# Kernel tuning notes

Measured on AMD Instinct MI355X. Metric: run time of the kernel, lower is better.

The kernel has to match this reference:

```python
import jax, jax.numpy as jnp
import numpy as np

N_NODES = 100000
N_EDGES = 1000000
EMB = 64
HID = 64
N_CLASSES = 1
LEAKY_SLOPE = 0.01  # flax.linen.leaky_relu default


def setup_inputs() -> dict:
    key = jax.random.key(0)
    k1, k2, k3, k4, k5 = jax.random.split(key, 5)
    node_ids = jnp.arange(N_NODES, dtype=jnp.int32)
    senders = jax.random.randint(k1, (N_EDGES,), 0, N_NODES, dtype=jnp.int32)
    receivers = jax.random.randint(k2, (N_EDGES,), 0, N_NODES, dtype=jnp.int32)
    embed_table = jax.random.normal(k3, (N_NODES, EMB), dtype=jnp.float32) * 0.05
    W1 = jax.random.normal(k4, (EMB, HID), dtype=jnp.float32) * (1.0 / np.sqrt(EMB))
    W2 = jax.random.normal(k5, (HID, N_CLASSES), dtype=jnp.float32) * (1.0 / np.sqrt(HID))
    b2 = jnp.zeros((N_CLASSES,), dtype=jnp.float32)
    return {"node_ids": node_ids, "senders": senders, "receivers": receivers,
            "embed_table": embed_table, "W1": W1, "W2": W2, "b2": b2}


def gcn_aggregate(x, senders, receivers, n_nodes, symmetric):
    # Faithful to jraph.GraphConvolution: update_node_fn is applied BEFORE this.
    if symmetric:
        ones = jnp.ones_like(senders, dtype=x.dtype)
        send_deg = jax.ops.segment_sum(ones, senders, num_segments=n_nodes)
        recv_deg = jax.ops.segment_sum(ones, receivers, num_segments=n_nodes)
        x = x * jax.lax.rsqrt(jnp.maximum(send_deg, 1.0))[:, None]
        x = jax.ops.segment_sum(x[senders], receivers, num_segments=n_nodes)  # [N, d]
        x = x * jax.lax.rsqrt(jnp.maximum(recv_deg, 1.0))[:, None]
    else:
        x = jax.ops.segment_sum(x[senders], receivers, num_segments=n_nodes)
    return x


def reference(node_ids, senders, receivers, embed_table, W1, W2, b2):
    n = node_ids.shape[0]
    # GraphMapFeatures(embed_node_fn=nn.Embed(...))
    x = embed_table[node_ids]                      # [N, EMB]
    # GraphConvolution(Dense(hidden, use_bias=False), symmetric_normalization=True)
    x = x @ W1                                     # [N, HID]
    x = gcn_aggregate(x, senders, receivers, n, symmetric=True)
    x = jax.nn.leaky_relu(x, negative_slope=LEAKY_SLOPE)
    # GraphConvolution(Dense(classes), symmetric_normalization=False)
    x = x @ W2 + b2                                # [N, C]
    x = gcn_aggregate(x, senders, receivers, n, symmetric=False)
    return jax.nn.sigmoid(x)
```

## Files before the change

kernel.cpp:

```cpp
#include <hip/hip_runtime.h>
#include <hip/hip_bf16.h>

#define N_NODES 100000
#define N_EDGES 1000000
#define SCAN_B 256
#define N_BLOCKS_RS ((N_NODES + 255) / 256)
#define N_BLOCKS_A  ((N_NODES + 63) / 64)

#define CHUNKS 40
#define CHUNK_E 25000
#define HWORDS 25000
#define HIST_BLOCKS (2 * CHUNKS)
#define MLP_BLOCKS 176
#define MLP_WAVES (MLP_BLOCKS * 16)


__device__ __forceinline__ unsigned f32_to_bf16(float v) {
    unsigned u = __float_as_uint(v);
    return (u + 0x7fffu + ((u >> 16) & 1u)) >> 16;
}

__global__ void k_hist8_mlp(const int4* __restrict__ s4,
                            const int4* __restrict__ r4,
                            unsigned* __restrict__ ghist_s8,
                            unsigned* __restrict__ ghist_r8,
                            unsigned char* __restrict__ rank8,
                            const float* __restrict__ emb,
                            const float* __restrict__ W1,
                            unsigned short* __restrict__ h16) {
    __shared__ unsigned lds[HWORDS];
    int b = blockIdx.x;
    int t = threadIdx.x;

    if (b >= HIST_BLOCKS) {
        int lane = t & 63;
        int gw   = (b - HIST_BLOCKS) * 16 + (t >> 6);
        float w1c[64];
#pragma unroll
        for (int k = 0; k < 64; ++k) w1c[k] = W1[k * 64 + lane];

        for (int n = gw; n < N_NODES; n += MLP_WAVES) {
            float e = emb[(size_t)n * 64 + lane];
            float a0 = 0.f, a1 = 0.f, a2 = 0.f, a3 = 0.f;
            int ei = __float_as_int(e);
#pragma unroll
            for (int k = 0; k < 16; ++k) {
                a0 += __int_as_float(__builtin_amdgcn_readlane(ei, 4 * k + 0)) * w1c[4 * k + 0];
                a1 += __int_as_float(__builtin_amdgcn_readlane(ei, 4 * k + 1)) * w1c[4 * k + 1];
                a2 += __int_as_float(__builtin_amdgcn_readlane(ei, 4 * k + 2)) * w1c[4 * k + 2];
                a3 += __int_as_float(__builtin_amdgcn_readlane(ei, 4 * k + 3)) * w1c[4 * k + 3];
            }
            float a = (a0 + a1) + (a2 + a3);
            h16[(size_t)n * 64 + lane] = (unsigned short)f32_to_bf16(a);
        }
        return;
    }

    int isR = (b < CHUNKS);
    int c   = isR ? b : b - CHUNKS;

    for (int w = t; w < HWORDS; w += 1024) lds[w] = 0u;
    __syncthreads();

    int beg = c * (CHUNK_E / 4);
    int end = beg + CHUNK_E / 4;
    if (isR) {
        for (int q = beg + t; q < end; q += 1024) {
            int4 v = r4[q];
            int sh0 = (v.x & 3) * 8, sh1 = (v.y & 3) * 8;
            int sh2 = (v.z & 3) * 8, sh3 = (v.w & 3) * 8;
            unsigned o0 = atomicAdd(&lds[v.x >> 2], 1u << sh0);
            unsigned o1 = atomicAdd(&lds[v.y >> 2], 1u << sh1);
            unsigned o2 = atomicAdd(&lds[v.z >> 2], 1u << sh2);
            unsigned o3 = atomicAdd(&lds[v.w >> 2], 1u << sh3);
            uchar4 rk;
            rk.x = (unsigned char)((o0 >> sh0) & 0xffu);
            rk.y = (unsigned char)((o1 >> sh1) & 0xffu);
            rk.z = (unsigned char)((o2 >> sh2) & 0xffu);
            rk.w = (unsigned char)((o3 >> sh3) & 0xffu);
            *(uchar4*)(rank8 + 4 * (size_t)q) = rk;
        }
    } else {
        for (int q = beg + t; q < end; q += 1024) {
            int4 v = s4[q];
            atomicAdd(&lds[v.x >> 2], 1u << ((v.x & 3) * 8));
            atomicAdd(&lds[v.y >> 2], 1u << ((v.y & 3) * 8));
            atomicAdd(&lds[v.z >> 2], 1u << ((v.z & 3) * 8));
            atomicAdd(&lds[v.w >> 2], 1u << ((v.w & 3) * 8));
        }
    }
    __syncthreads();

    uint4* __restrict__ dst =
        (uint4*)((isR ? ghist_r8 : ghist_s8) + (size_t)c * HWORDS);
    const uint4* lsrc = (const uint4*)lds;
    for (int w = t; w < HWORDS / 4; w += 1024) dst[w] = lsrc[w];
}

__global__ void k_scanA(const unsigned char* __restrict__ gs8,
                        const unsigned char* __restrict__ gr8,
                        unsigned char* __restrict__ base8,
                        int* __restrict__ part,
                        float* __restrict__ rs,
                        int* __restrict__ blockSums) {
    __shared__ int s[64];
    int t = threadIdx.x;
    int g = t >> 2, sl = t & 3;
    int node = blockIdx.x * 64 + g;
    int total = 0;
    if (node < N_NODES) {
        unsigned ss = 0;
#pragma unroll
        for (int k = 0; k < 10; ++k)
            ss += gs8[(size_t)(sl * 10 + k) * N_NODES + node];
        ss += __shfl_xor(ss, 1, 64);
        ss += __shfl_xor(ss, 2, 64);
        if (sl == 0) rs[node] = rsqrtf(fmaxf((float)ss, 1.0f));

        unsigned rv[10];
        unsigned rsum = 0;
#pragma unroll
        for (int k = 0; k < 10; ++k) {
            rv[k] = gr8[(size_t)(sl * 10 + k) * N_NODES + node];
            rsum += rv[k];
        }
        unsigned x = rsum;
        unsigned u1 = __shfl_up(x, 1, 4); if (sl >= 1) x += u1;
        unsigned u2 = __shfl_up(x, 2, 4); if (sl >= 2) x += u2;
        unsigned run = x - rsum;
        total = (int)__shfl(x, 3, 4);
#pragma unroll
        for (int k = 0; k < 10; ++k) {
            base8[(size_t)(sl * 10 + k) * N_NODES + node] = (unsigned char)run;
            run += rv[k];
        }
    }
    if (sl == 0) s[g] = total;
    __syncthreads();
    if (t < 64) {
        int v = s[t];
        int acc = v;
#pragma unroll
        for (int off = 1; off < 64; off <<= 1) {
            int y = __shfl_up(acc, off, 64);
            if (t >= off) acc += y;
        }
        s[t] = acc - v;
        if (t == 63) blockSums[blockIdx.x] = acc;
    }
    __syncthreads();
    if (sl == 0 && node < N_NODES) part[node] = s[g];
}

__global__ void k_rows(const int* __restrict__ part,
                       const int* __restrict__ blockSums,
                       int* __restrict__ row_start) {
    __shared__ int s[SCAN_B];
    __shared__ int gsum[4];
    int t = threadIdx.x;
    int b = blockIdx.x;

    int acc = 0;
    for (int j = t; j < 4 * b; j += SCAN_B) acc += blockSums[j];
    s[t] = acc;
    __syncthreads();
    for (int off = SCAN_B / 2; off > 0; off >>= 1) {
        if (t < off) s[t] += s[t + off];
        __syncthreads();
    }
    int blockOff = s[0];
    if (t < 4)
        gsum[t] = (4 * b + t < N_BLOCKS_A) ? blockSums[4 * b + t] : 0;
    __syncthreads();

    int gi = t >> 6;
    int goff = blockOff;
    if (gi > 0) goff += gsum[0];
    if (gi > 1) goff += gsum[1];
    if (gi > 2) goff += gsum[2];
    int n = b * SCAN_B + t;
    if (n < N_NODES) row_start[n] = goff + part[n];
    if (b == 0 && t == 0) row_start[N_NODES] = N_EDGES;
}

__global__ void k_fill(const int4* __restrict__ s4,
                       const int4* __restrict__ r4,
                       const uchar4* __restrict__ rk4,
                       const unsigned char* __restrict__ base8,
                       const int* __restrict__ row_start,
                       int* __restrict__ col) {
    int i = blockIdx.x * blockDim.x + threadIdx.x;
    if (i >= N_EDGES / 4) return;
    int c = (4 * i) / CHUNK_E;
    const unsigned char* __restrict__ bs = base8 + (size_t)c * N_NODES;
    int4 s = s4[i];
    int4 r = r4[i];
    uchar4 rk = rk4[i];
    col[row_start[r.x] + bs[r.x] + rk.x] = s.x;
    col[row_start[r.y] + bs[r.y] + rk.y] = s.y;
    col[row_start[r.z] + bs[r.z] + rk.z] = s.z;
    col[row_start[r.w] + bs[r.w] + rk.w] = s.w;
}

__global__ void k_agg_post(const int* __restrict__ row_start,
                           const int* __restrict__ col,
                           const uint4* __restrict__ h128,
                           const float* __restrict__ rs,
                           const float* __restrict__ W2,
                           const float* __restrict__ b2,
                           float* __restrict__ z) {
    int wid  = (blockIdx.x * blockDim.x + threadIdx.x) >> 6;
    int lane = threadIdx.x & 63;
    if (wid >= N_NODES) return;
    int eslot = lane >> 3;
    int fq    = lane & 7;

    int start = row_start[wid];
    int end   = row_start[wid + 1];
    float a0 = 0.f, a1 = 0.f, a2 = 0.f, a3 = 0.f;
    float a4 = 0.f, a5 = 0.f, a6 = 0.f, a7 = 0.f;
    for (int i = start + eslot; i < end; i += 8) {
        int sx = col[i];
        float rss = rs[sx];
        uint4 u = h128[(size_t)sx * 8 + fq];
        a0 += rss * __uint_as_float(u.x << 16);
        a1 += rss * __uint_as_float(u.x & 0xffff0000u);
        a2 += rss * __uint_as_float(u.y << 16);
        a3 += rss * __uint_as_float(u.y & 0xffff0000u);
        a4 += rss * __uint_as_float(u.z << 16);
        a5 += rss * __uint_as_float(u.z & 0xffff0000u);
        a6 += rss * __uint_as_float(u.w << 16);
        a7 += rss * __uint_as_float(u.w & 0xffff0000u);
    }
#pragma unroll
    for (int off = 8; off < 64; off <<= 1) {
        a0 += __shfl_xor(a0, off, 64);
        a1 += __shfl_xor(a1, off, 64);
        a2 += __shfl_xor(a2, off, 64);
        a3 += __shfl_xor(a3, off, 64);
        a4 += __shfl_xor(a4, off, 64);
        a5 += __shfl_xor(a5, off, 64);
        a6 += __shfl_xor(a6, off, 64);
        a7 += __shfl_xor(a7, off, 64);
    }
    float rsq = rsqrtf(fmaxf((float)(end - start), 1.0f));
    float4 wA = ((const float4*)W2)[fq * 2];
    float4 wB = ((const float4*)W2)[fq * 2 + 1];
    float p = 0.f, x;
    x = a0 * rsq; x = (x > 0.f) ? x : 0.01f * x; p += x * wA.x;
    x = a1 * rsq; x = (x > 0.f) ? x : 0.01f * x; p += x * wA.y;
    x = a2 * rsq; x = (x > 0.f) ? x : 0.01f * x; p += x * wA.z;
    x = a3 * rsq; x = (x > 0.f) ? x : 0.01f * x; p += x * wA.w;
    x = a4 * rsq; x = (x > 0.f) ? x : 0.01f * x; p += x * wB.x;
    x = a5 * rsq; x = (x > 0.f) ? x : 0.01f * x; p += x * wB.y;
    x = a6 * rsq; x = (x > 0.f) ? x : 0.01f * x; p += x * wB.z;
    x = a7 * rsq; x = (x > 0.f) ? x : 0.01f * x; p += x * wB.w;
    p += __shfl_xor(p, 1, 64);
    p += __shfl_xor(p, 2, 64);
    p += __shfl_xor(p, 4, 64);
    if (lane == 0) z[wid] = p + b2[0];
}

__global__ void k_agg2_sigmoid(const int* __restrict__ row_start,
                               const int* __restrict__ col,
                               const float* __restrict__ z,
                               float* __restrict__ out) {
    int gtid = blockIdx.x * blockDim.x + threadIdx.x;
    int n  = gtid >> 2;
    int sl = gtid & 3;
    if (n >= N_NODES) return;
    int start = row_start[n];
    int end   = row_start[n + 1];
    float acc = 0.f;
    for (int i = start + sl; i < end; i += 4) acc += z[col[i]];
    acc += __shfl_xor(acc, 1, 64);
    acc += __shfl_xor(acc, 2, 64);
    if (sl == 0) out[n] = 1.0f / (1.0f + expf(-acc));
}

extern "C" void kernel_launch(void* const* d_in, const int* in_sizes, int n_in,
                              void* d_out, int out_size, void* d_ws, size_t ws_size,
                              hipStream_t stream) {
    const int* senders    = (const int*)d_in[1];
    const int* receivers  = (const int*)d_in[2];
    const float* emb      = (const float*)d_in[3];
    const float* W1       = (const float*)d_in[4];
    const float* W2       = (const float*)d_in[5];
    const float* b2       = (const float*)d_in[6];
    float* out            = (float*)d_out;

    char* ws = (char*)d_ws;
    unsigned char*  ghist_s8  = (unsigned char*)(ws);
    unsigned char*  ghist_r8  = (unsigned char*)(ws + 4000000);
    unsigned char*  base8     = (unsigned char*)(ws + 8000000);
    unsigned char*  rank8     = (unsigned char*)(ws + 12000000);
    int*            part      = (int*)(ws + 13000000);
    int*            row_start = (int*)(ws + 13400000);
    int*            blockSums = (int*)(ws + 13800016);
    float*          rs        = (float*)(ws + 13807600);
    int*            col       = (int*)(ws + 14207600);
    unsigned short* h16       = (unsigned short*)(ws + 18207616);
    float*          z         = (float*)(ws + 31007616);

    const int B = 256;
    const int QBLK = (N_EDGES / 4 + B - 1) / B;

    k_hist8_mlp<<<HIST_BLOCKS + MLP_BLOCKS, 1024, 0, stream>>>(
        (const int4*)senders, (const int4*)receivers,
        (unsigned*)ghist_s8, (unsigned*)ghist_r8, rank8, emb, W1, h16);
    k_scanA<<<N_BLOCKS_A, B, 0, stream>>>(
        ghist_s8, ghist_r8, base8, part, rs, blockSums);
    k_rows<<<N_BLOCKS_RS, SCAN_B, 0, stream>>>(part, blockSums, row_start);
    k_fill<<<QBLK, B, 0, stream>>>(
        (const int4*)senders, (const int4*)receivers,
        (const uchar4*)rank8, base8, row_start, col);
    k_agg_post<<<(N_NODES * 64) / B, B, 0, stream>>>(
        row_start, col, (const uint4*)h16, rs, W2, b2, z);
    k_agg2_sigmoid<<<(N_NODES * 4 + B - 1) / B, B, 0, stream>>>(
        row_start, col, z, out);
}
```

Before: 190.1 us.

## Fuse CSR build stages into one cooperative kernel with grid syncs

Merges the histogram/MLP, scan, row-offset and fill kernels into a single cooperative kernel of 256 blocks that uses grid.sync between phases, removing three kernel launches and their inter-kernel gaps. The scan is restructured so each lane handles a whole node across all 40 chunks, followed by a single-block scan of group sums. The fill phase computes offsets from groupOff+part directly instead of reading row_start. The risks are grid-sync overhead, the fixed 256-block grid limiting parallelism for the fill, and the requirement that all blocks be co-resident.

Result: slower. 299.3 us (+57.5%).

```diff
diff --git a/kernel.cpp b/kernel.cpp
--- a/kernel.cpp
+++ b/kernel.cpp
@@ -1,11 +1,11 @@
 #include <hip/hip_runtime.h>
+#include <hip/hip_cooperative_groups.h>
 #include <hip/hip_bf16.h>
+
+namespace cg = cooperative_groups;
 
 #define N_NODES 100000
 #define N_EDGES 1000000
-#define SCAN_B 256
-#define N_BLOCKS_RS ((N_NODES + 255) / 256)
-#define N_BLOCKS_A  ((N_NODES + 63) / 64)
 
 #define CHUNKS 40
 #define CHUNK_E 25000
@@ -13,6 +13,8 @@
 #define HIST_BLOCKS (2 * CHUNKS)
 #define MLP_BLOCKS 176
 #define MLP_WAVES (MLP_BLOCKS * 16)
+#define NG 1563
+#define GRID_THREADS (256 * 1024)
 
 
 __device__ __forceinline__ unsigned f32_to_bf16(float v) {
@@ -20,25 +22,65 @@
     return (u + 0x7fffu + ((u >> 16) & 1u)) >> 16;
 }
 
-__global__ void k_hist8_mlp(const int4* __restrict__ s4,
-                            const int4* __restrict__ r4,
-                            unsigned* __restrict__ ghist_s8,
-                            unsigned* __restrict__ ghist_r8,
-                            unsigned char* __restrict__ rank8,
-                            const float* __restrict__ emb,
-                            const float* __restrict__ W1,
-                            unsigned short* __restrict__ h16) {
-    __shared__ unsigned lds[HWORDS];
+__global__ void __launch_bounds__(1024, 1)
+k_build(const int4* __restrict__ s4, const int4* __restrict__ r4,
+        unsigned char* __restrict__ ghist_s8,
+        unsigned char* __restrict__ ghist_r8,
+        unsigned char* __restrict__ rank8,
+        const float* __restrict__ emb, const float* __restrict__ W1,
+        unsigned short* __restrict__ h16,
+        unsigned char* __restrict__ base8,
+        int* __restrict__ part, float* __restrict__ rs,
+        int* __restrict__ blockSums, int* __restrict__ groupOff,
+        int* __restrict__ row_start, int* __restrict__ col) {
+    __shared__ unsigned lds[HWORDS + 600];
+    cg::grid_group grid = cg::this_grid();
     int b = blockIdx.x;
     int t = threadIdx.x;
 
-    if (b >= HIST_BLOCKS) {
+    if (b < HIST_BLOCKS) {
+        int isR = (b < CHUNKS);
+        int c   = isR ? b : b - CHUNKS;
+        for (int w = t; w < HWORDS; w += 1024) lds[w] = 0u;
+        __syncthreads();
+        int beg = c * (CHUNK_E / 4);
+        int end = beg + CHUNK_E / 4;
+        if (isR) {
+            for (int q = beg + t; q < end; q += 1024) {
+                int4 v = r4[q];
+                int sh0 = (v.x & 3) * 8, sh1 = (v.y & 3) * 8;
+                int sh2 = (v.z & 3) * 8, sh3 = (v.w & 3) * 8;
+                unsigned o0 = atomicAdd(&lds[v.x >> 2], 1u << sh0);
+                unsigned o1 = atomicAdd(&lds[v.y >> 2], 1u << sh1);
+                unsigned o2 = atomicAdd(&lds[v.z >> 2], 1u << sh2);
+                unsigned o3 = atomicAdd(&lds[v.w >> 2], 1u << sh3);
+                uchar4 rk;
+                rk.x = (unsigned char)((o0 >> sh0) & 0xffu);
+                rk.y = (unsigned char)((o1 >> sh1) & 0xffu);
+                rk.z = (unsigned char)((o2 >> sh2) & 0xffu);
+                rk.w = (unsigned char)((o3 >> sh3) & 0xffu);
+                *(uchar4*)(rank8 + 4 * (size_t)q) = rk;
+            }
+        } else {
+            for (int q = beg + t; q < end; q += 1024) {
+                int4 v = s4[q];
+                atomicAdd(&lds[v.x >> 2], 1u << ((v.x & 3) * 8));
+                atomicAdd(&lds[v.y >> 2], 1u << ((v.y & 3) * 8));
+                atomicAdd(&lds[v.z >> 2], 1u << ((v.z & 3) * 8));
+                atomicAdd(&lds[v.w >> 2], 1u << ((v.w & 3) * 8));
+            }
+        }
+        __syncthreads();
+        uint4* __restrict__ dst =
+            (uint4*)((isR ? ghist_r8 : ghist_s8) + (size_t)c * HWORDS * 4);
+        const uint4* lsrc = (const uint4*)lds;
+        for (int w = t; w < HWORDS / 4; w += 1024) dst[w] = lsrc[w];
+    } else {
         int lane = t & 63;
         int gw   = (b - HIST_BLOCKS) * 16 + (t >> 6);
         float w1c[64];
 #pragma unroll
         for (int k = 0; k < 64; ++k) w1c[k] = W1[k * 64 + lane];
-
         for (int n = gw; n < N_NODES; n += MLP_WAVES) {
             float e = emb[(size_t)n * 64 + lane];
             float a0 = 0.f, a1 = 0.f, a2 = 0.f, a3 = 0.f;
@@ -53,153 +95,74 @@
             float a = (a0 + a1) + (a2 + a3);
             h16[(size_t)n * 64 + lane] = (unsigned short)f32_to_bf16(a);
         }
-        return;
-    }
-
-    int isR = (b < CHUNKS);
-    int c   = isR ? b : b - CHUNKS;
-
-    for (int w = t; w < HWORDS; w += 1024) lds[w] = 0u;
-    __syncthreads();
-
-    int beg = c * (CHUNK_E / 4);
-    int end = beg + CHUNK_E / 4;
-    if (isR) {
-        for (int q = beg + t; q < end; q += 1024) {
-            int4 v = r4[q];
-            int sh0 = (v.x & 3) * 8, sh1 = (v.y & 3) * 8;
-            int sh2 = (v.z & 3) * 8, sh3 = (v.w & 3) * 8;
-            unsigned o0 = atomicAdd(&lds[v.x >> 2], 1u << sh0);
-            unsigned o1 = atomicAdd(&lds[v.y >> 2], 1u << sh1);
-            unsigned o2 = atomicAdd(&lds[v.z >> 2], 1u << sh2);
-            unsigned o3 = atomicAdd(&lds[v.w >> 2], 1u << sh3);
-            uchar4 rk;
-            rk.x = (unsigned char)((o0 >> sh0) & 0xffu);
-            rk.y = (unsigned char)((o1 >> sh1) & 0xffu);
-            rk.z = (unsigned char)((o2 >> sh2) & 0xffu);
-            rk.w = (unsigned char)((o3 >> sh3) & 0xffu);
-            *(uchar4*)(rank8 + 4 * (size_t)q) = rk;
-        }
-    } else {
-        for (int q = beg + t; q < end; q += 1024) {
-            int4 v = s4[q];
-            atomicAdd(&lds[v.x >> 2], 1u << ((v.x & 3) * 8));
-            atomicAdd(&lds[v.y >> 2], 1u << ((v.y & 3) * 8));
-            atomicAdd(&lds[v.z >> 2], 1u << ((v.z & 3) * 8));
-            atomicAdd(&lds[v.w >> 2], 1u << ((v.w & 3) * 8));
-        }
-    }
-    __syncthreads();
-
-    uint4* __restrict__ dst =
-        (uint4*)((isR ? ghist_r8 : ghist_s8) + (size_t)c * HWORDS);
-    const uint4* lsrc = (const uint4*)lds;
-    for (int w = t; w < HWORDS / 4; w += 1024) dst[w] = lsrc[w];
-}
-
-__global__ void k_scanA(const unsigned char* __restrict__ gs8,
-                        const unsigned char* __restrict__ gr8,
-                        unsigned char* __restrict__ base8,
-                        int* __restrict__ part,
-                        float* __restrict__ rs,
-                        int* __restrict__ blockSums) {
-    __shared__ int s[64];
-    int t = threadIdx.x;
-    int g = t >> 2, sl = t & 3;
-    int node = blockIdx.x * 64 + g;
-    int total = 0;
-    if (node < N_NODES) {
-        unsigned ss = 0;
-#pragma unroll
-        for (int k = 0; k < 10; ++k)
-            ss += gs8[(size_t)(sl * 10 + k) * N_NODES + node];
-        ss += __shfl_xor(ss, 1, 64);
-        ss += __shfl_xor(ss, 2, 64);
-        if (sl == 0) rs[node] = rsqrtf(fmaxf((float)ss, 1.0f));
-
-        unsigned rv[10];
-        unsigned rsum = 0;
-#pragma unroll
-        for (int k = 0; k < 10; ++k) {
-            rv[k] = gr8[(size_t)(sl * 10 + k) * N_NODES + node];
-            rsum += rv[k];
-        }
-        unsigned x = rsum;
-        unsigned u1 = __shfl_up(x, 1, 4); if (sl >= 1) x += u1;
-        unsigned u2 = __shfl_up(x, 2, 4); if (sl >= 2) x += u2;
-        unsigned run = x - rsum;
-        total = (int)__shfl(x, 3, 4);
-#pragma unroll
-        for (int k = 0; k < 10; ++k) {
-            base8[(size_t)(sl * 10 + k) * N_NODES + node] = (unsigned char)run;
-            run += rv[k];
-        }
-    }
-    if (sl == 0) s[g] = total;
-    __syncthreads();
-    if (t < 64) {
-        int v = s[t];
-        int acc = v;
-#pragma unroll
-        for (int off = 1; off < 64; off <<= 1) {
-            int y = __shfl_up(acc, off, 64);
-            if (t >= off) acc += y;
-        }
-        s[t] = acc - v;
-        if (t == 63) blockSums[blockIdx.x] = acc;
-    }
-    __syncthreads();
-    if (sl == 0 && node < N_NODES) part[node] = s[g];
-}
-
-__global__ void k_rows(const int* __restrict__ part,
-                       const int* __restrict__ blockSums,
-                       int* __restrict__ row_start) {
-    __shared__ int s[SCAN_B];
-    __shared__ int gsum[4];
-    int t = threadIdx.x;
-    int b = blockIdx.x;
-
-    int acc = 0;
-    for (int j = t; j < 4 * b; j += SCAN_B) acc += blockSums[j];
-    s[t] = acc;
-    __syncthreads();
-    for (int off = SCAN_B / 2; off > 0; off >>= 1) {
-        if (t < off) s[t] += s[t + off];
+    }
+    grid.sync();
+
+    {
+        int wv   = b * 16 + (t >> 6);
+        int lane = t & 63;
+        if (wv < NG) {
+            int node = wv * 64 + lane;
+            int total = 0;
+            if (node < N_NODES) {
+                unsigned ss = 0;
+#pragma unroll
+                for (int c = 0; c < CHUNKS; ++c)
+                    ss += ghist_s8[(size_t)c * N_NODES + node];
+                rs[node] = rsqrtf(fmaxf((float)ss, 1.0f));
+                unsigned run = 0;
+#pragma unroll
+                for (int c = 0; c < CHUNKS; ++c) {
+                    unsigned v = ghist_r8[(size_t)c * N_NODES + node];
+                    base8[(size_t)c * N_NODES + node] = (unsigned char)run;
+                    run += v;
+                }
+                total = (int)run;
+            }
+            int acc = total;
+#pragma unroll
+            for (int off = 1; off < 64; off <<= 1) {
+                int y = __shfl_up(acc, off, 64);
+                if (lane >= off) acc += y;
+            }
+            if (node < N_NODES) part[node] = acc - total;
+            if (lane == 63) blockSums[wv] = acc;
+        }
+    }
+    grid.sync();
+
+    if (b == 0) {
+        int* A = (int*)lds;
+        int* Bb = A + 2048;
+        for (int j = t; j < 2048; j += 1024) A[j] = (j < NG) ? blockSums[j] : 0;
         __syncthreads();
-    }
-    int blockOff = s[0];
-    if (t < 4)
-        gsum[t] = (4 * b + t < N_BLOCKS_A) ? blockSums[4 * b + t] : 0;
-    __syncthreads();
-
-    int gi = t >> 6;
-    int goff = blockOff;
-    if (gi > 0) goff += gsum[0];
-    if (gi > 1) goff += gsum[1];
-    if (gi > 2) goff += gsum[2];
-    int n = b * SCAN_B + t;
-    if (n < N_NODES) row_start[n] = goff + part[n];
-    if (b == 0 && t == 0) row_start[N_NODES] = N_EDGES;
-}
-
-__global__ void k_fill(const int4* __restrict__ s4,
-                       const int4* __restrict__ r4,
-                       const uchar4* __restrict__ rk4,
-                       const unsigned char* __restrict__ base8,
-                       const int* __restrict__ row_start,
-                       int* __restrict__ col) {
-    int i = blockIdx.x * blockDim.x + threadIdx.x;
-    if (i >= N_EDGES / 4) return;
-    int c = (4 * i) / CHUNK_E;
-    const unsigned char* __restrict__ bs = base8 + (size_t)c * N_NODES;
-    int4 s = s4[i];
-    int4 r = r4[i];
-    uchar4 rk = rk4[i];
-    col[row_start[r.x] + bs[r.x] + rk.x] = s.x;
-    col[row_start[r.y] + bs[r.y] + rk.y] = s.y;
-    col[row_start[r.z] + bs[r.z] + rk.z] = s.z;
-    col[row_start[r.w] + bs[r.w] + rk.w] = s.w;
+        int* src = A;
+        int* dst = Bb;
+        for (int off = 1; off < 2048; off <<= 1) {
+            for (int j = t; j < 2048; j += 1024)
+                dst[j] = src[j] + ((j >= off) ? src[j - off] : 0);
+            __syncthreads();
+            int* tmp = src; src = dst; dst = tmp;
+        }
+        for (int j = t; j < NG; j += 1024)
+            groupOff[j] = j ? src[j - 1] : 0;
+    }
+    grid.sync();
+
+    int gtid = b * 1024 + t;
+    for (int n = gtid; n <= N_NODES; n += GRID_THREADS)
+        row_start[n] = (n < N_NODES) ? groupOff[n >> 6] + part[n] : N_EDGES;
+    for (int i = gtid; i < N_EDGES / 4; i += GRID_THREADS) {
+        int c = (4 * i) / CHUNK_E;
+        const unsigned char* __restrict__ bs = base8 + (size_t)c * N_NODES;
+        int4 s = s4[i];
+        int4 r = r4[i];
+        uchar4 rk = *(const uchar4*)(rank8 + 4 * (size_t)i);
+        col[groupOff[r.x >> 6] + part[r.x] + bs[r.x] + rk.x] = s.x;
+        col[groupOff[r.y >> 6] + part[r.y] + bs[r.y] + rk.y] = s.y;
+        col[groupOff[r.z >> 6] + part[r.z] + bs[r.z] + rk.z] = s.z;
+        col[groupOff[r.w >> 6] + part[r.w] + bs[r.w] + rk.w] = s.w;
+    }
 }
 
 __global__ void k_agg_post(const int* __restrict__ row_start,
@@ -281,13 +244,13 @@
 extern "C" void kernel_launch(void* const* d_in, const int* in_sizes, int n_in,
                               void* d_out, int out_size, void* d_ws, size_t ws_size,
                               hipStream_t stream) {
-    const int* senders    = (const int*)d_in[1];
-    const int* receivers  = (const int*)d_in[2];
-    const float* emb      = (const float*)d_in[3];
-    const float* W1       = (const float*)d_in[4];
-    const float* W2       = (const float*)d_in[5];
-    const float* b2       = (const float*)d_in[6];
-    float* out            = (float*)d_out;
+    const int4*  s4p  = (const int4*)d_in[1];
+    const int4*  r4p  = (const int4*)d_in[2];
+    const float* emb  = (const float*)d_in[3];
+    const float* W1   = (const float*)d_in[4];
+    const float* W2   = (const float*)d_in[5];
+    const float* b2   = (const float*)d_in[6];
+    float* out        = (float*)d_out;
 
     char* ws = (char*)d_ws;
     unsigned char*  ghist_s8  = (unsigned char*)(ws);
@@ -297,25 +260,20 @@
     int*            part      = (int*)(ws + 13000000);
     int*            row_start = (int*)(ws + 13400000);
     int*            blockSums = (int*)(ws + 13800016);
-    float*          rs        = (float*)(ws + 13807600);
-    int*            col       = (int*)(ws + 14207600);
-    unsigned short* h16       = (unsigned short*)(ws + 18207616);
-    float*          z         = (float*)(ws + 31007616);
-
-    const int B = 256;
-    const int QBLK = (N_EDGES / 4 + B - 1) / B;
-
-    k_hist8_mlp<<<HIST_BLOCKS + MLP_BLOCKS, 1024, 0, stream>>>(
-        (const int4*)senders, (const int4*)receivers,
-        (unsigned*)ghist_s8, (unsigned*)ghist_r8, rank8, emb, W1, h16);
-    k_scanA<<<N_BLOCKS_A, B, 0, stream>>>(
-        ghist_s8, ghist_r8, base8, part, rs, blockSums);
-    k_rows<<<N_BLOCKS_RS, SCAN_B, 0, stream>>>(part, blockSums, row_start);
-    k_fill<<<QBLK, B, 0, stream>>>(
-        (const int4*)senders, (const int4*)receivers,
-        (const uchar4*)rank8, base8, row_start, col);
-    k_agg_post<<<(N_NODES * 64) / B, B, 0, stream>>>(
+    int*            groupOff  = (int*)(ws + 13806272);
+    float*          rs        = (float*)(ws + 13812544);
+    int*            col       = (int*)(ws + 14212544);
+    unsigned short* h16       = (unsigned short*)(ws + 18212544);
+    float*          z         = (float*)(ws + 31012544);
+
+    void* args[] = {
+        (void*)&s4p, (void*)&r4p, (void*)&ghist_s8, (void*)&ghist_r8,
+        (void*)&rank8, (void*)&emb, (void*)&W1, (void*)&h16,
+        (void*)&base8, (void*)&part, (void*)&rs, (void*)&blockSums,
+        (void*)&groupOff, (void*)&row_start, (void*)&col };
+    hipLaunchCooperativeKernel((void*)k_build, dim3(256), dim3(1024),
+                               args, 0, stream);
+    k_agg_post<<<25000, 256, 0, stream>>>(
         row_start, col, (const uint4*)h16, rs, W2, b2, z);
-    k_agg2_sigmoid<<<(N_NODES * 4 + B - 1) / B, B, 0, stream>>>(
-        row_start, col, z, out);
-}
+    k_agg2_sigmoid<<<1563, 256, 0, stream>>>(row_start, col, z, out);
+}
```

## Quantize hidden features to int8 with per-node scale and prefetch first gather iterations

Applied to the files above, without the earlier changes.

Hidden features after the first dense layer are stored as int8 with a per-row absmax scale instead of bf16. The scale is folded into the sender normalization factor in the scan kernel. This halves gather traffic in the aggregation kernel at the cost of extra quantization error. Both aggregation kernels also peel their first two edge iterations to issue loads early, and the second aggregation uses 8 lanes per node instead of 4.

Result: slower. 199.7 us (+5.1%).

```diff
diff --git a/kernel.cpp b/kernel.cpp
--- a/kernel.cpp
+++ b/kernel.cpp
@@ -10,24 +10,25 @@
 #define CHUNKS 40
 #define CHUNK_E 25000
 #define HWORDS 25000
+#define CPL 10
 #define HIST_BLOCKS (2 * CHUNKS)
 #define MLP_BLOCKS 176
 #define MLP_WAVES (MLP_BLOCKS * 16)
 
 
-__device__ __forceinline__ unsigned f32_to_bf16(float v) {
-    unsigned u = __float_as_uint(v);
-    return (u + 0x7fffu + ((u >> 16) & 1u)) >> 16;
-}
-
-__global__ void k_hist8_mlp(const int4* __restrict__ s4,
-                            const int4* __restrict__ r4,
-                            unsigned* __restrict__ ghist_s8,
-                            unsigned* __restrict__ ghist_r8,
-                            unsigned char* __restrict__ rank8,
-                            const float* __restrict__ emb,
-                            const float* __restrict__ W1,
-                            unsigned short* __restrict__ h16) {
+__device__ __forceinline__ float sb(unsigned w, int k) {
+    return (float)((signed char)((w >> (8 * k)) & 0xffu));
+}
+
+__global__ void k_hist_mlp(const int4* __restrict__ s4,
+                           const int4* __restrict__ r4,
+                           unsigned* __restrict__ ghist_s8,
+                           unsigned* __restrict__ ghist_r8,
+                           unsigned char* __restrict__ rank8,
+                           const float* __restrict__ emb,
+                           const float* __restrict__ W1,
+                           signed char* __restrict__ h8,
+                           float* __restrict__ scale) {
     __shared__ unsigned lds[HWORDS];
     int b = blockIdx.x;
     int t = threadIdx.x;
@@ -51,7 +52,14 @@
                 a3 += __int_as_float(__builtin_amdgcn_readlane(ei, 4 * k + 3)) * w1c[4 * k + 3];
             }
             float a = (a0 + a1) + (a2 + a3);
-            h16[(size_t)n * 64 + lane] = (unsigned short)f32_to_bf16(a);
+            float mx = fabsf(a);
+#pragma unroll
+            for (int off = 1; off < 64; off <<= 1)
+                mx = fmaxf(mx, __shfl_xor(mx, off, 64));
+            mx = fmaxf(mx, 1e-20f);
+            int q = (int)rintf(a * (127.0f / mx));
+            h8[(size_t)n * 64 + lane] = (signed char)q;
+            if (lane == 0) scale[n] = mx * (1.0f / 127.0f);
         }
         return;
     }
@@ -101,7 +109,8 @@
                         const unsigned char* __restrict__ gr8,
                         unsigned char* __restrict__ base8,
                         int* __restrict__ part,
-                        float* __restrict__ rs,
+                        const float* __restrict__ scale,
+                        float* __restrict__ hsc,
                         int* __restrict__ blockSums) {
     __shared__ int s[64];
     int t = threadIdx.x;
@@ -111,17 +120,18 @@
     if (node < N_NODES) {
         unsigned ss = 0;
 #pragma unroll
-        for (int k = 0; k < 10; ++k)
-            ss += gs8[(size_t)(sl * 10 + k) * N_NODES + node];
+        for (int k = 0; k < CPL; ++k)
+            ss += gs8[(size_t)(sl * CPL + k) * N_NODES + node];
         ss += __shfl_xor(ss, 1, 64);
         ss += __shfl_xor(ss, 2, 64);
-        if (sl == 0) rs[node] = rsqrtf(fmaxf((float)ss, 1.0f));
-
-        unsigned rv[10];
+        if (sl == 0)
+            hsc[node] = scale[node] * rsqrtf(fmaxf((float)ss, 1.0f));
+
+        unsigned rv[CPL];
         unsigned rsum = 0;
 #pragma unroll
-        for (int k = 0; k < 10; ++k) {
-            rv[k] = gr8[(size_t)(sl * 10 + k) * N_NODES + node];
+        for (int k = 0; k < CPL; ++k) {
+            rv[k] = gr8[(size_t)(sl * CPL + k) * N_NODES + node];
             rsum += rv[k];
         }
         unsigned x = rsum;
@@ -130,8 +140,8 @@
         unsigned run = x - rsum;
         total = (int)__shfl(x, 3, 4);
 #pragma unroll
-        for (int k = 0; k < 10; ++k) {
-            base8[(size_t)(sl * 10 + k) * N_NODES + node] = (unsigned char)run;
+        for (int k = 0; k < CPL; ++k) {
+            base8[(size_t)(sl * CPL + k) * N_NODES + node] = (unsigned char)run;
             run += rv[k];
         }
     }
@@ -204,8 +214,8 @@
 
 __global__ void k_agg_post(const int* __restrict__ row_start,
                            const int* __restrict__ col,
-                           const uint4* __restrict__ h128,
-                           const float* __restrict__ rs,
+                           const uint2* __restrict__ h8v,
+                           const float* __restrict__ hsc,
                            const float* __restrict__ W2,
                            const float* __restrict__ b2,
                            float* __restrict__ z) {
@@ -217,20 +227,39 @@
 
     int start = row_start[wid];
     int end   = row_start[wid + 1];
-    float a0 = 0.f, a1 = 0.f, a2 = 0.f, a3 = 0.f;
-    float a4 = 0.f, a5 = 0.f, a6 = 0.f, a7 = 0.f;
-    for (int i = start + eslot; i < end; i += 8) {
+    int i0 = start + eslot;
+    int i1 = i0 + 8;
+    bool p0 = i0 < end, p1 = i1 < end;
+    int c0 = p0 ? col[i0] : 0;
+    int c1 = p1 ? col[i1] : 0;
+    float hs0 = hsc[c0];
+    float hs1 = hsc[c1];
+    uint2 u0 = h8v[(size_t)c0 * 8 + fq];
+    uint2 u1 = h8v[(size_t)c1 * 8 + fq];
+    if (!p0) { u0.x = 0u; u0.y = 0u; }
+    if (!p1) { u1.x = 0u; u1.y = 0u; }
+
+    float a0 = hs0 * sb(u0.x, 0) + hs1 * sb(u1.x, 0);
+    float a1 = hs0 * sb(u0.x, 1) + hs1 * sb(u1.x, 1);
+    float a2 = hs0 * sb(u0.x, 2) + hs1 * sb(u1.x, 2);
+    float a3 = hs0 * sb(u0.x, 3) + hs1 * sb(u1.x, 3);
+    float a4 = hs0 * sb(u0.y, 0) + hs1 * sb(u1.y, 0);
+    float a5 = hs0 * sb(u0.y, 1) + hs1 * sb(u1.y, 1);
+    float a6 = hs0 * sb(u0.y, 2) + hs1 * sb(u1.y, 2);
+    float a7 = hs0 * sb(u0.y, 3) + hs1 * sb(u1.y, 3);
+
+    for (int i = i1 + 8; i < end; i += 8) {
         int sx = col[i];
-        float rss = rs[sx];
-        uint4 u = h128[(size_t)sx * 8 + fq];
-        a0 += rss * __uint_as_float(u.x << 16);
-        a1 += rss * __uint_as_float(u.x & 0xffff0000u);
-        a2 += rss * __uint_as_float(u.y << 16);
-        a3 += rss * __uint_as_float(u.y & 0xffff0000u);
-        a4 += rss * __uint_as_float(u.z << 16);
-        a5 += rss * __uint_as_float(u.z & 0xffff0000u);
-        a6 += rss * __uint_as_float(u.w << 16);
-        a7 += rss * __uint_as_float(u.w & 0xffff0000u);
+        float hs = hsc[sx];
+        uint2 u = h8v[(size_t)sx * 8 + fq];
+        a0 += hs * sb(u.x, 0);
+        a1 += hs * sb(u.x, 1);
+        a2 += hs * sb(u.x, 2);
+        a3 += hs * sb(u.x, 3);
+        a4 += hs * sb(u.y, 0);
+        a5 += hs * sb(u.y, 1);
+        a6 += hs * sb(u.y, 2);
+        a7 += hs * sb(u.y, 3);
     }
 #pragma unroll
     for (int off = 8; off < 64; off <<= 1) {
@@ -244,17 +273,16 @@
         a7 += __shfl_xor(a7, off, 64);
     }
     float rsq = rsqrtf(fmaxf((float)(end - start), 1.0f));
-    float4 wA = ((const float4*)W2)[fq * 2];
-    float4 wB = ((const float4*)W2)[fq * 2 + 1];
+    const float* __restrict__ w2p = W2 + 8 * fq;
     float p = 0.f, x;
-    x = a0 * rsq; x = (x > 0.f) ? x : 0.01f * x; p += x * wA.x;
-    x = a1 * rsq; x = (x > 0.f) ? x : 0.01f * x; p += x * wA.y;
-    x = a2 * rsq; x = (x > 0.f) ? x : 0.01f * x; p += x * wA.z;
-    x = a3 * rsq; x = (x > 0.f) ? x : 0.01f * x; p += x * wA.w;
-    x = a4 * rsq; x = (x > 0.f) ? x : 0.01f * x; p += x * wB.x;
-    x = a5 * rsq; x = (x > 0.f) ? x : 0.01f * x; p += x * wB.y;
-    x = a6 * rsq; x = (x > 0.f) ? x : 0.01f * x; p += x * wB.z;
-    x = a7 * rsq; x = (x > 0.f) ? x : 0.01f * x; p += x * wB.w;
+    x = a0 * rsq; x = (x > 0.f) ? x : 0.01f * x; p += x * w2p[0];
+    x = a1 * rsq; x = (x > 0.f) ? x : 0.01f * x; p += x * w2p[1];
+    x = a2 * rsq; x = (x > 0.f) ? x : 0.01f * x; p += x * w2p[2];
+    x = a3 * rsq; x = (x > 0.f) ? x : 0.01f * x; p += x * w2p[3];
+    x = a4 * rsq; x = (x > 0.f) ? x : 0.01f * x; p += x * w2p[4];
+    x = a5 * rsq; x = (x > 0.f) ? x : 0.01f * x; p += x * w2p[5];
+    x = a6 * rsq; x = (x > 0.f) ? x : 0.01f * x; p += x * w2p[6];
+    x = a7 * rsq; x = (x > 0.f) ? x : 0.01f * x; p += x * w2p[7];
     p += __shfl_xor(p, 1, 64);
     p += __shfl_xor(p, 2, 64);
     p += __shfl_xor(p, 4, 64);
@@ -266,15 +294,23 @@
                                const float* __restrict__ z,
                                float* __restrict__ out) {
     int gtid = blockIdx.x * blockDim.x + threadIdx.x;
-    int n  = gtid >> 2;
-    int sl = gtid & 3;
+    int n  = gtid >> 3;
+    int sl = gtid & 7;
     if (n >= N_NODES) return;
     int start = row_start[n];
     int end   = row_start[n + 1];
-    float acc = 0.f;
-    for (int i = start + sl; i < end; i += 4) acc += z[col[i]];
+    int i0 = start + sl;
+    int i1 = i0 + 8;
+    bool p0 = i0 < end, p1 = i1 < end;
+    int c0 = p0 ? col[i0] : 0;
+    int c1 = p1 ? col[i1] : 0;
+    float z0 = z[c0];
+    float z1 = z[c1];
+    float acc = (p0 ? z0 : 0.f) + (p1 ? z1 : 0.f);
+    for (int i = i1 + 8; i < end; i += 8) acc += z[col[i]];
     acc += __shfl_xor(acc, 1, 64);
     acc += __shfl_xor(acc, 2, 64);
+    acc += __shfl_xor(acc, 4, 64);
     if (sl == 0) out[n] = 1.0f / (1.0f + expf(-acc));
 }
 
@@ -297,25 +333,26 @@
     int*            part      = (int*)(ws + 13000000);
     int*            row_start = (int*)(ws + 13400000);
     int*            blockSums = (int*)(ws + 13800016);
-    float*          rs        = (float*)(ws + 13807600);
-    int*            col       = (int*)(ws + 14207600);
-    unsigned short* h16       = (unsigned short*)(ws + 18207616);
-    float*          z         = (float*)(ws + 31007616);
+    float*          scale     = (float*)(ws + 13806272);
+    float*          hsc       = (float*)(ws + 14206272);
+    int*            col       = (int*)(ws + 14606272);
+    signed char*    h8        = (signed char*)(ws + 18606336);
+    float*          z         = (float*)(ws + 25006336);
 
     const int B = 256;
     const int QBLK = (N_EDGES / 4 + B - 1) / B;
 
-    k_hist8_mlp<<<HIST_BLOCKS + MLP_BLOCKS, 1024, 0, stream>>>(
+    k_hist_mlp<<<HIST_BLOCKS + MLP_BLOCKS, 1024, 0, stream>>>(
         (const int4*)senders, (const int4*)receivers,
-        (unsigned*)ghist_s8, (unsigned*)ghist_r8, rank8, emb, W1, h16);
+        (unsigned*)ghist_s8, (unsigned*)ghist_r8, rank8, emb, W1, h8, scale);
     k_scanA<<<N_BLOCKS_A, B, 0, stream>>>(
-        ghist_s8, ghist_r8, base8, part, rs, blockSums);
+        ghist_s8, ghist_r8, base8, part, scale, hsc, blockSums);
     k_rows<<<N_BLOCKS_RS, SCAN_B, 0, stream>>>(part, blockSums, row_start);
     k_fill<<<QBLK, B, 0, stream>>>(
         (const int4*)senders, (const int4*)receivers,
         (const uchar4*)rank8, base8, row_start, col);
     k_agg_post<<<(N_NODES * 64) / B, B, 0, stream>>>(
-        row_start, col, (const uint4*)h16, rs, W2, b2, z);
-    k_agg2_sigmoid<<<(N_NODES * 4 + B - 1) / B, B, 0, stream>>>(
+        row_start, col, (const uint2*)h8, hsc, W2, b2, z);
+    k_agg2_sigmoid<<<(N_NODES * 8 + B - 1) / B, B, 0, stream>>>(
         row_start, col, z, out);
 }
```
